# Kernel optimization log

Measured on AMD Instinct MI355X. Metric: run time of the kernel, lower is better.

## Reference

```python
import jax, jax.numpy as jnp
import numpy as np

NUM_ATOMS = 100
D = 32        # initial_atom_dim
H = 16        # hidden_dim (multiplicity per irrep)
NB = 16       # edge_dim / number of bessel basis functions
CUT = 6.0     # radius_cutoff
DEG = 4.0     # degree_norm
OUT = 1       # output_dim
INV4PI = 1.0 / np.sqrt(4.0 * np.pi)  # 'integral' SH normalization


def _bessel(d, nb, cut):
    # e3nn soft_one_hot_linspace(basis='bessel', cutoff=True) * sqrt(nb)
    x = d[:, None]
    n = jnp.arange(1, nb + 1, dtype=d.dtype)
    safe = jnp.maximum(x, 1e-9)
    out = np.sqrt(2.0 / cut) * jnp.sin(n * jnp.pi * x / cut) / safe
    return out * (x < cut) * np.sqrt(float(nb))


def _fc(x, w1, w2):
    # e3nn FullyConnectedNet: fan-in normalized linear layers, silu, no bias
    h = jax.nn.silu(x @ w1 / np.sqrt(x.shape[-1]))
    return h @ w2 / np.sqrt(w1.shape[-1])


def _forward(atomic_numbers, edge_index, coords, atom_emb,
             fc0_w1, fc0_w2, fc1_w1, fc1_w2, w_readout):
    src, dst = edge_index[0], edge_index[1]
    N = coords.shape[0]
    E = src.shape[0]

    vec = coords[src] - coords[dst]                      # [E,3]
    dist = jnp.linalg.norm(vec, axis=-1)                 # [E]
    unit = vec / jnp.maximum(dist, 1e-9)[:, None]

    # spherical harmonics, l=0 and l=1, 'integral' normalization
    y0 = jnp.full((E,), INV4PI, dtype=coords.dtype)      # [E]
    y1 = (np.sqrt(3.0) * INV4PI) * unit                  # [E,3]
    basis = _bessel(dist, NB, CUT)                       # [E,NB]

    x = atom_emb[atomic_numbers]                         # [N,D] (row 0 is padding)

    # ---- layer 0: scalars (D x0e) x (1x0e+1x1o) -> H x0e + H x1o ----
    w = _fc(basis, fc0_w1, fc0_w2)                       # [E, 2*D*H] per-edge TP weights
    wa = w[:, : D * H].reshape(E, D, H)
    wb = w[:, D * H:].reshape(E, D, H)
    xs = x[src]
    n0 = 1.0 / np.sqrt(D)                                # path fan-in norm
    m0 = jnp.einsum('ed,edh->eh', xs, wa) * y0[:, None] * n0          # [E,H]
    m1 = jnp.einsum('ed,edh->eh', xs, wb)[:, :, None] * y1[:, None, :] * n0  # [E,H,3]
    z0 = jax.ops.segment_sum(m0, dst, num_segments=N) / DEG           # [N,H]
    z1 = jax.ops.segment_sum(m1, dst, num_segments=N) / DEG           # [N,H,3]

    # ---- layer 1: (H x0e + H x1o) x (1x0e+1x1o) -> same irreps, skip-connected ----
    w = _fc(basis, fc1_w1, fc1_w2)                       # [E, 4*H*H]
    w1_ = w[:, 0 * H * H:1 * H * H].reshape(E, H, H)     # 0e x 0e -> 0e
    w2_ = w[:, 1 * H * H:2 * H * H].reshape(E, H, H)     # 0e x 1o -> 1o
    w3_ = w[:, 2 * H * H:3 * H * H].reshape(E, H, H)     # 1o x 0e -> 1o
    w4_ = w[:, 3 * H * H:4 * H * H].reshape(E, H, H)     # 1o x 1o -> 0e (CG = dot/sqrt(3))
    s, v = z0[src], z1[src]
    n1 = 1.0 / np.sqrt(2 * H)                            # two paths per output irrep
    dot = jnp.einsum('ehm,em->eh', v, y1) / np.sqrt(3.0)
    o0 = (jnp.einsum('eh,ehk->ek', s, w1_) * y0[:, None]
          + jnp.einsum('eh,ehk->ek', dot, w4_)) * n1
    o1 = (jnp.einsum('eh,ehk->ek', s, w2_)[:, :, None] * y1[:, None, :]
          + jnp.einsum('ehm,ehk->ekm', v, w3_) * y0[:, None, None]) * n1
    z0 = jax.ops.segment_sum(o0, dst, num_segments=N) / DEG + z0      # skip
    z1 = jax.ops.segment_sum(o1, dst, num_segments=N) / DEG + z1

    # ---- scalar readout (o3.Linear onto 0e) + graph sum-pool ----
    node_scalar = z0 @ w_readout / np.sqrt(H)            # [N,OUT]
    return jnp.sum(node_scalar, axis=0)                  # [OUT]


def setup_inputs() -> dict:
    key = jax.random.key(0)
    ks = jax.random.split(key, 9)
    N, E = 10000, 160000
    atomic_numbers = jax.random.randint(ks[0], (N,), 0, NUM_ATOMS)
    coords = jax.random.normal(ks[1], (N, 3), dtype=jnp.float32)
    edge_index = jax.random.randint(ks[2], (2, E), 0, N)
    atom_emb = jax.random.normal(ks[3], (NUM_ATOMS, D), dtype=jnp.float32).at[0].set(0.0)
    fc0_w1 = jax.random.normal(ks[4], (NB, H), dtype=jnp.float32)
    fc0_w2 = jax.random.normal(ks[5], (H, 2 * D * H), dtype=jnp.float32)
    fc1_w1 = jax.random.normal(ks[6], (NB, H), dtype=jnp.float32)
    fc1_w2 = jax.random.normal(ks[7], (H, 4 * H * H), dtype=jnp.float32)
    w_readout = jax.random.normal(ks[8], (H, OUT), dtype=jnp.float32)
    return {"atomic_numbers": atomic_numbers, "coords": coords, "edge_index": edge_index,
            "atom_emb": atom_emb, "fc0_w1": fc0_w1, "fc0_w2": fc0_w2,
            "fc1_w1": fc1_w1, "fc1_w2": fc1_w2, "w_readout": w_readout}


def reference(atomic_numbers, coords, edge_index, atom_emb,
              fc0_w1, fc0_w2, fc1_w1, fc1_w2, w_readout):
    return _forward(atomic_numbers, edge_index, coords, atom_emb,
                    fc0_w1, fc0_w2, fc1_w1, fc1_w2, w_readout)
```

## Files before the change

### kernel.cpp

```cpp
#include <hip/hip_runtime.h>
#include <math.h>


namespace {
constexpr int   NATOMS   = 100;
constexpr int   CAP      = 64;
constexpr float PI_F     = 3.14159265358979323846f;
constexpr float INV4PI_F = 0.28209479177387814f;
constexpr float SQRT3_F  = 1.7320508075688772f;
constexpr float CUT_F    = 6.0f;
constexpr float BASIS_C  = 2.3094010767585034f;
constexpr float N0_F     = 0.17677669529663687f;
constexpr float K0_F = INV4PI_F * N0_F * 0.0625f;
constexpr float K1_F = SQRT3_F * INV4PI_F * N0_F * 0.0625f;
constexpr float P2SC = INV4PI_F * N0_F * (1.0f / 64.0f);
}

__device__ __forceinline__ float silu_fast(float x) {
  return x / (1.0f + __expf(-x));
}

__device__ __forceinline__ float block_reduce_sum(float v) {
  #pragma unroll
  for (int o = 32; o > 0; o >>= 1) v += __shfl_down(v, o, 64);
  __shared__ float ls[8];
  int lane = threadIdx.x & 63;
  int w    = threadIdx.x >> 6;
  if (lane == 0) ls[w] = v;
  __syncthreads();
  float s = 0.f;
  if (threadIdx.x == 0) {
    int nw = (blockDim.x + 63) >> 6;
    for (int i = 0; i < nw; ++i) s += ls[i];
  }
  return s;
}

__global__ void table_kernel(const float* __restrict__ atom_emb,
                             const float* __restrict__ fc0_w2,
                             const float* __restrict__ fc1_w2,
                             const float* __restrict__ w_readout,
                             float* __restrict__ TI,
                             float* __restrict__ G1T, float* __restrict__ G4T,
                             int* __restrict__ dcur,
                             float* __restrict__ out,
                             int N2) {
  int b = blockIdx.x;
  int tt = threadIdx.x;
  if (b < NATOMS) {
    int j = tt >> 4;
    int h = tt & 15;
    float s0 = 0.f, s1 = 0.f;
    #pragma unroll
    for (int d = 0; d < 32; ++d) {
      float x = atom_emb[b * 32 + d];
      s0 = fmaf(x, fc0_w2[j * 1024 + d * 16 + h], s0);
      s1 = fmaf(x, fc0_w2[j * 1024 + 512 + d * 16 + h], s1);
    }
    TI[b * 512 + j * 32 + 2 * h]     = s0;
    TI[b * 512 + j * 32 + 2 * h + 1] = s1;
  } else if (b == NATOMS) {
    int j = tt >> 4;
    int h = tt & 15;
    float g1 = 0.f, g4 = 0.f;
    #pragma unroll
    for (int k = 0; k < 16; ++k) {
      float r = w_readout[k];
      g1 = fmaf(fc1_w2[j * 1024 + h * 16 + k], r, g1);
      g4 = fmaf(fc1_w2[j * 1024 + 768 + h * 16 + k], r, g4);
    }
    G1T[h * 16 + j] = g1;
    G4T[h * 16 + j] = g4;
    if (tt == 0) *out = 0.f;
  } else {
    int idx = (b - NATOMS - 1) * 256 + tt;
    if (idx < N2) dcur[idx] = 0;
  }
}

__global__ void __launch_bounds__(256)
edge_kernel(const int* __restrict__ ei,
            const float* __restrict__ coords,
            const int* __restrict__ an,
            const float* __restrict__ TI,
            const float* __restrict__ fc0_w1,
            const float* __restrict__ fc1_w1,
            int* __restrict__ dcur, int* __restrict__ scur,
            float2* __restrict__ mbuf,
            float4* __restrict__ ubuf,
            float4* __restrict__ sbuf,
            float* __restrict__ hbuf,
            int E) {
  int lane = threadIdx.x & 63;
  int g    = threadIdx.x >> 4;
  int t    = threadIdx.x & 15;
  int base = lane & 48;

  float w0c[16], w1c[16];
  #pragma unroll
  for (int k = 0; k < 16; ++k) {
    w0c[k] = fc0_w1[k * 16 + t];
    w1c[k] = fc1_w1[k * 16 + t];
  }

  const float angc = PI_F / CUT_F;
  int eA = blockIdx.x * 32 + g;
  int eB = eA + 16;
  bool vA = eA < E, vB = eB < E;
  int eAc = vA ? eA : 0, eBc = vB ? eB : 0;

  int sA = ei[eAc], dA = ei[E + eAc];
  int sB = ei[eBc], dB = ei[E + eBc];
  float sxA = coords[3 * sA + 0], syA = coords[3 * sA + 1], szA = coords[3 * sA + 2];
  float dxA = coords[3 * dA + 0], dyA = coords[3 * dA + 1], dzA = coords[3 * dA + 2];
  float sxB = coords[3 * sB + 0], syB = coords[3 * sB + 1], szB = coords[3 * sB + 2];
  float dxB = coords[3 * dB + 0], dyB = coords[3 * dB + 1], dzB = coords[3 * dB + 2];
  int aA = an[sA], aB = an[sB];

  float vxA = sxA - dxA, vyA = syA - dyA, vzA = szA - dzA;
  float vxB = sxB - dxB, vyB = syB - dyB, vzB = szB - dzB;
  float distA = sqrtf(vxA * vxA + vyA * vyA + vzA * vzA);
  float distB = sqrtf(vxB * vxB + vyB * vyB + vzB * vzB);
  float ivA = 1.0f / fmaxf(distA, 1e-9f);
  float ivB = 1.0f / fmaxf(distB, 1e-9f);
  float uxA = vxA * ivA, uyA = vyA * ivA, uzA = vzA * ivA;
  float uxB = vxB * ivB, uyB = vyB * ivB, uzB = vzB * ivB;
  float bcA = (distA < CUT_F) ? (BASIS_C * ivA) : 0.0f;
  float bcB = (distB < CUT_F) ? (BASIS_C * ivB) : 0.0f;

  int dsAv = 0, ssAv = 0, dsBv = 0, ssBv = 0;
  if (t == 0) {
    if (vA) {
      int p = atomicAdd(&dcur[dA], 1), q = atomicAdd(&scur[sA], 1);
      dsAv = dA * CAP + min(p, CAP - 1);
      ssAv = sA * CAP + min(q, CAP - 1);
      ubuf[dsAv] = make_float4(uxA, uyA, uzA, distA);
      sbuf[ssAv] = make_float4(uxA, uyA, uzA, distA);
    }
    if (vB) {
      int p = atomicAdd(&dcur[dB], 1), q = atomicAdd(&scur[sB], 1);
      dsBv = dB * CAP + min(p, CAP - 1);
      ssBv = sB * CAP + min(q, CAP - 1);
      ubuf[dsBv] = make_float4(uxB, uyB, uzB, distB);
      sbuf[ssBv] = make_float4(uxB, uyB, uzB, distB);
    }
  }

  float angA = angc * distA, angB = angc * distB;
  float scA = __sinf(angA), twA = 2.0f * __cosf(angA), spA = 0.f;
  float scB = __sinf(angB), twB = 2.0f * __cosf(angB), spB = 0.f;
  float a0A = 0.f, a1A = 0.f, a0B = 0.f, a1B = 0.f;
  #pragma unroll
  for (int k = 0; k < 16; ++k) {
    a0A = fmaf(scA, w0c[k], a0A);
    a1A = fmaf(scA, w1c[k], a1A);
    a0B = fmaf(scB, w0c[k], a0B);
    a1B = fmaf(scB, w1c[k], a1B);
    float snA = fmaf(twA, scA, -spA); spA = scA; scA = snA;
    float snB = fmaf(twB, scB, -spB); spB = scB; scB = snB;
  }
  float h0A = silu_fast(a0A * bcA * 0.25f);
  float h1A = silu_fast(a1A * bcA * 0.25f);
  float h0B = silu_fast(a0B * bcB * 0.25f);
  float h1B = silu_fast(a1B * bcB * 0.25f);

  int dsA = __shfl(dsAv, base, 64);
  int ssA = __shfl(ssAv, base, 64);
  int dsB = __shfl(dsBv, base, 64);
  int ssB = __shfl(ssBv, base, 64);

  const float2* tpA = (const float2*)(TI + aA * 512) + t;
  const float2* tpB = (const float2*)(TI + aB * 512) + t;
  float u0A = 0.f, u1A = 0.f, u0B = 0.f, u1B = 0.f;
  #pragma unroll
  for (int j = 0; j < 16; ++j) {
    float hjA = __shfl(h0A, base + j, 64);
    float hjB = __shfl(h0B, base + j, 64);
    float2 TA = tpA[j * 16];
    float2 TB = tpB[j * 16];
    u0A = fmaf(hjA, TA.x, u0A);
    u1A = fmaf(hjA, TA.y, u1A);
    u0B = fmaf(hjB, TB.x, u0B);
    u1B = fmaf(hjB, TB.y, u1B);
  }

  if (vA) {
    hbuf[(size_t)ssA * 16 + t] = h1A;
    mbuf[(size_t)dsA * 16 + t] = make_float2(K0_F * u0A, K1_F * u1A);
  }
  if (vB) {
    hbuf[(size_t)ssB * 16 + t] = h1B;
    mbuf[(size_t)dsB * 16 + t] = make_float2(K0_F * u0B, K1_F * u1B);
  }
}

__global__ void __launch_bounds__(256, 4)
node_kernel(const int* __restrict__ dcur,
            const int* __restrict__ scur,
            const float2* __restrict__ mbuf,
            const float4* __restrict__ ubuf,
            const float4* __restrict__ sbuf,
            const float* __restrict__ hbuf,
            const float* __restrict__ G1T,
            const float* __restrict__ G4T,
            const float* __restrict__ w_readout,
            float* __restrict__ out,
            int N) {
  __shared__ float ggs[512];
  ggs[threadIdx.x]       = G1T[threadIdx.x];
  ggs[256 + threadIdx.x] = G4T[threadIdx.x];
  __syncthreads();

  int wave = threadIdx.x >> 6;
  int lane = threadIdx.x & 63;
  int g    = lane >> 4;
  int t    = lane & 15;
  int base = lane & 48;
  int node = blockIdx.x * 4 + wave;
  bool valid = node < N;

  float rr = w_readout[t];
  int cin  = valid ? min(dcur[node], CAP) : 0;
  int cout = valid ? min(scur[node], CAP) : 0;
  size_t nb = (size_t)(valid ? node : 0) * CAP;

  float a0 = 0.f, ax = 0.f, ay = 0.f, az = 0.f;
  for (int i = g; i < cin; i += 4) {
    float2 f  = mbuf[(nb + i) * 16 + t];
    float4 uu = ubuf[nb + i];
    a0 += f.x;
    ax = fmaf(f.y, uu.x, ax);
    ay = fmaf(f.y, uu.y, ay);
    az = fmaf(f.y, uu.z, az);
  }
  a0 += __shfl_xor(a0, 16, 64); a0 += __shfl_xor(a0, 32, 64);
  ax += __shfl_xor(ax, 16, 64); ax += __shfl_xor(ax, 32, 64);
  ay += __shfl_xor(ay, 16, 64); ay += __shfl_xor(ay, 32, 64);
  az += __shfl_xor(az, 16, 64); az += __shfl_xor(az, 32, 64);

  float srcv = (g == 0) ? a0 : ((g == 1) ? ax : (g == 2) ? ay : az);
  int tofs = (g == 0) ? 0 : 256;
  float o = 0.f;
  #pragma unroll
  for (int h = 0; h < 16; ++h) {
    float vh = __shfl(srcv, base + h, 64);
    o = fmaf(ggs[tofs + h * 16 + t], vh, o);
  }
  float Qt  = __shfl(o, t, 64);
  float Pxt = __shfl(o, 16 + t, 64);
  float Pyt = __shfl(o, 32 + t, 64);
  float Pzt = __shfl(o, 48 + t, 64);

  float c = 0.f;
  for (int i = g; i < cout; i += 4) {
    float h1 = hbuf[(nb + i) * 16 + t];
    float4 uu = sbuf[nb + i];
    c = fmaf(h1, fmaf(Pxt, uu.x, fmaf(Pyt, uu.y, fmaf(Pzt, uu.z, Qt))), c);
  }
  c *= P2SC;
  if (valid && g == 0) c = fmaf(a0 * rr, 0.25f, c);
  if (!valid) c = 0.f;

  float tot = block_reduce_sum(c);
  if (threadIdx.x == 0) atomicAdd(out, tot);
}

extern "C" void kernel_launch(void* const* d_in, const int* in_sizes, int n_in,
                              void* d_out, int out_size, void* d_ws, size_t ws_size,
                              hipStream_t stream) {
  const int*   an        = (const int*)d_in[0];
  const float* coords    = (const float*)d_in[1];
  const int*   ei        = (const int*)d_in[2];
  const float* atom_emb  = (const float*)d_in[3];
  const float* fc0_w1    = (const float*)d_in[4];
  const float* fc0_w2    = (const float*)d_in[5];
  const float* fc1_w1    = (const float*)d_in[6];
  const float* fc1_w2    = (const float*)d_in[7];
  const float* w_readout = (const float*)d_in[8];

  int N = in_sizes[0];
  int E = in_sizes[2] / 2;
  size_t slots = (size_t)N * CAP;

  float4* ubuf = (float4*)d_ws;
  float4* sbuf = ubuf + slots;
  float2* mbuf = (float2*)(sbuf + slots);
  float*  hbuf = (float*)(mbuf + slots * 16);
  float*  TI   = hbuf + slots * 16;
  float*  G1T  = TI + NATOMS * 512;
  float*  G4T  = G1T + 256;
  int*    dcur = (int*)(G4T + 256);
  int*    scur = dcur + N;
  float*  out = (float*)d_out;

  int blk = 256;
  int zgrid = (2 * N + blk - 1) / blk;
  table_kernel<<<NATOMS + 1 + zgrid, blk, 0, stream>>>(
      atom_emb, fc0_w2, fc1_w2, w_readout, TI, G1T, G4T, dcur, out, 2 * N);

  edge_kernel<<<(E + 31) / 32, blk, 0, stream>>>(
      ei, coords, an, TI, fc0_w1, fc1_w1, dcur, scur,
      mbuf, ubuf, sbuf, hbuf, E);

  node_kernel<<<(N + 3) / 4, blk, 0, stream>>>(
      dcur, scur, mbuf, ubuf, sbuf, hbuf, G1T, G4T, w_readout, out, N);
}
```

Baseline: 148.6 us.

## Replace bucketed edge slots with float atomics and a separate edge readout pass

Drops the per-node fixed-capacity bucket lists built with integer atomic counters. Edge messages are now scatter-added straight into per-node accumulators with float atomics, and a new node kernel computes per-node Q/P vectors. A second edge pass then gathers those vectors by source index to form the readout. This removes the CAP=64 truncation and the large sparse slot buffers, at the cost of many more float atomics and an extra kernel launch with a random gather.

```diff
diff --git a/kernel.cpp b/kernel.cpp
--- a/kernel.cpp
+++ b/kernel.cpp
@@ -4,7 +4,6 @@
 
 namespace {
 constexpr int   NATOMS   = 100;
-constexpr int   CAP      = 64;
 constexpr float PI_F     = 3.14159265358979323846f;
 constexpr float INV4PI_F = 0.28209479177387814f;
 constexpr float SQRT3_F  = 1.7320508075688772f;
@@ -42,9 +41,9 @@
                              const float* __restrict__ w_readout,
                              float* __restrict__ TI,
                              float* __restrict__ G1T, float* __restrict__ G4T,
-                             int* __restrict__ dcur,
+                             float* __restrict__ zacc,
                              float* __restrict__ out,
-                             int N2) {
+                             int N64) {
   int b = blockIdx.x;
   int tt = threadIdx.x;
   if (b < NATOMS) {
@@ -74,7 +73,7 @@
     if (tt == 0) *out = 0.f;
   } else {
     int idx = (b - NATOMS - 1) * 256 + tt;
-    if (idx < N2) dcur[idx] = 0;
+    if (idx < N64) zacc[idx] = 0.f;
   }
 }
 
@@ -85,11 +84,9 @@
             const float* __restrict__ TI,
             const float* __restrict__ fc0_w1,
             const float* __restrict__ fc1_w1,
-            int* __restrict__ dcur, int* __restrict__ scur,
-            float2* __restrict__ mbuf,
+            float* __restrict__ zacc,
+            float* __restrict__ hbuf,
             float4* __restrict__ ubuf,
-            float4* __restrict__ sbuf,
-            float* __restrict__ hbuf,
             int E) {
   int lane = threadIdx.x & 63;
   int g    = threadIdx.x >> 4;
@@ -128,22 +125,9 @@
   float bcA = (distA < CUT_F) ? (BASIS_C * ivA) : 0.0f;
   float bcB = (distB < CUT_F) ? (BASIS_C * ivB) : 0.0f;
 
-  int dsAv = 0, ssAv = 0, dsBv = 0, ssBv = 0;
   if (t == 0) {
-    if (vA) {
-      int p = atomicAdd(&dcur[dA], 1), q = atomicAdd(&scur[sA], 1);
-      dsAv = dA * CAP + min(p, CAP - 1);
-      ssAv = sA * CAP + min(q, CAP - 1);
-      ubuf[dsAv] = make_float4(uxA, uyA, uzA, distA);
-      sbuf[ssAv] = make_float4(uxA, uyA, uzA, distA);
-    }
-    if (vB) {
-      int p = atomicAdd(&dcur[dB], 1), q = atomicAdd(&scur[sB], 1);
-      dsBv = dB * CAP + min(p, CAP - 1);
-      ssBv = sB * CAP + min(q, CAP - 1);
-      ubuf[dsBv] = make_float4(uxB, uyB, uzB, distB);
-      sbuf[ssBv] = make_float4(uxB, uyB, uzB, distB);
-    }
+    if (vA) ubuf[eA] = make_float4(uxA, uyA, uzA, 0.f);
+    if (vB) ubuf[eB] = make_float4(uxB, uyB, uzB, 0.f);
   }
 
   float angA = angc * distA, angB = angc * distB;
@@ -164,10 +148,8 @@
   float h0B = silu_fast(a0B * bcB * 0.25f);
   float h1B = silu_fast(a1B * bcB * 0.25f);
 
-  int dsA = __shfl(dsAv, base, 64);
-  int ssA = __shfl(ssAv, base, 64);
-  int dsB = __shfl(dsBv, base, 64);
-  int ssB = __shfl(ssBv, base, 64);
+  if (vA) hbuf[(size_t)eA * 16 + t] = h1A;
+  if (vB) hbuf[(size_t)eB * 16 + t] = h1B;
 
   const float2* tpA = (const float2*)(TI + aA * 512) + t;
   const float2* tpB = (const float2*)(TI + aB * 512) + t;
@@ -185,82 +167,98 @@
   }
 
   if (vA) {
-    hbuf[(size_t)ssA * 16 + t] = h1A;
-    mbuf[(size_t)dsA * 16 + t] = make_float2(K0_F * u0A, K1_F * u1A);
+    float* za = zacc + (size_t)dA * 64 + t;
+    float m1 = K1_F * u1A;
+    unsafeAtomicAdd(za,      K0_F * u0A);
+    unsafeAtomicAdd(za + 16, m1 * uxA);
+    unsafeAtomicAdd(za + 32, m1 * uyA);
+    unsafeAtomicAdd(za + 48, m1 * uzA);
   }
   if (vB) {
-    hbuf[(size_t)ssB * 16 + t] = h1B;
-    mbuf[(size_t)dsB * 16 + t] = make_float2(K0_F * u0B, K1_F * u1B);
-  }
-}
-
-__global__ void __launch_bounds__(256, 4)
-node_kernel(const int* __restrict__ dcur,
-            const int* __restrict__ scur,
-            const float2* __restrict__ mbuf,
-            const float4* __restrict__ ubuf,
-            const float4* __restrict__ sbuf,
-            const float* __restrict__ hbuf,
-            const float* __restrict__ G1T,
-            const float* __restrict__ G4T,
-            const float* __restrict__ w_readout,
-            float* __restrict__ out,
-            int N) {
+    float* zb = zacc + (size_t)dB * 64 + t;
+    float m1 = K1_F * u1B;
+    unsafeAtomicAdd(zb,      K0_F * u0B);
+    unsafeAtomicAdd(zb + 16, m1 * uxB);
+    unsafeAtomicAdd(zb + 32, m1 * uyB);
+    unsafeAtomicAdd(zb + 48, m1 * uzB);
+  }
+}
+
+__global__ void __launch_bounds__(256)
+node_qp_kernel(const float* __restrict__ zacc,
+               const float* __restrict__ G1T,
+               const float* __restrict__ G4T,
+               const float* __restrict__ w_readout,
+               float* __restrict__ QP,
+               float* __restrict__ out,
+               int N) {
   __shared__ float ggs[512];
   ggs[threadIdx.x]       = G1T[threadIdx.x];
   ggs[256 + threadIdx.x] = G4T[threadIdx.x];
   __syncthreads();
 
-  int wave = threadIdx.x >> 6;
   int lane = threadIdx.x & 63;
-  int g    = lane >> 4;
   int t    = lane & 15;
   int base = lane & 48;
-  int node = blockIdx.x * 4 + wave;
+  int node = blockIdx.x * 16 + (threadIdx.x >> 4);
   bool valid = node < N;
-
-  float rr = w_readout[t];
-  int cin  = valid ? min(dcur[node], CAP) : 0;
-  int cout = valid ? min(scur[node], CAP) : 0;
-  size_t nb = (size_t)(valid ? node : 0) * CAP;
-
-  float a0 = 0.f, ax = 0.f, ay = 0.f, az = 0.f;
-  for (int i = g; i < cin; i += 4) {
-    float2 f  = mbuf[(nb + i) * 16 + t];
-    float4 uu = ubuf[nb + i];
-    a0 += f.x;
-    ax = fmaf(f.y, uu.x, ax);
-    ay = fmaf(f.y, uu.y, ay);
-    az = fmaf(f.y, uu.z, az);
-  }
-  a0 += __shfl_xor(a0, 16, 64); a0 += __shfl_xor(a0, 32, 64);
-  ax += __shfl_xor(ax, 16, 64); ax += __shfl_xor(ax, 32, 64);
-  ay += __shfl_xor(ay, 16, 64); ay += __shfl_xor(ay, 32, 64);
-  az += __shfl_xor(az, 16, 64); az += __shfl_xor(az, 32, 64);
-
-  float srcv = (g == 0) ? a0 : ((g == 1) ? ax : (g == 2) ? ay : az);
-  int tofs = (g == 0) ? 0 : 256;
-  float o = 0.f;
+  size_t nb = (size_t)(valid ? node : 0) * 64;
+
+  float z0 = zacc[nb + t];
+  float zx = zacc[nb + 16 + t];
+  float zy = zacc[nb + 32 + t];
+  float zz = zacc[nb + 48 + t];
+
+  float Q = 0.f, Px = 0.f, Py = 0.f, Pz = 0.f;
   #pragma unroll
   for (int h = 0; h < 16; ++h) {
-    float vh = __shfl(srcv, base + h, 64);
-    o = fmaf(ggs[tofs + h * 16 + t], vh, o);
-  }
-  float Qt  = __shfl(o, t, 64);
-  float Pxt = __shfl(o, 16 + t, 64);
-  float Pyt = __shfl(o, 32 + t, 64);
-  float Pzt = __shfl(o, 48 + t, 64);
+    float z0h = __shfl(z0, base + h, 64);
+    float zxh = __shfl(zx, base + h, 64);
+    float zyh = __shfl(zy, base + h, 64);
+    float zzh = __shfl(zz, base + h, 64);
+    float g1 = ggs[h * 16 + t];
+    float g4 = ggs[256 + h * 16 + t];
+    Q  = fmaf(g1, z0h, Q);
+    Px = fmaf(g4, zxh, Px);
+    Py = fmaf(g4, zyh, Py);
+    Pz = fmaf(g4, zzh, Pz);
+  }
+  if (valid) {
+    QP[nb + t]      = Q;
+    QP[nb + 16 + t] = Px;
+    QP[nb + 32 + t] = Py;
+    QP[nb + 48 + t] = Pz;
+  }
+
+  float c = valid ? 0.25f * z0 * w_readout[t] : 0.f;
+  float tot = block_reduce_sum(c);
+  if (threadIdx.x == 0) atomicAdd(out, tot);
+}
+
+__global__ void __launch_bounds__(256)
+edge2_kernel(const int* __restrict__ ei,
+             const float4* __restrict__ ubuf,
+             const float* __restrict__ hbuf,
+             const float* __restrict__ QP,
+             float* __restrict__ out,
+             int E) {
+  int t  = threadIdx.x & 15;
+  int gg = blockIdx.x * 16 + (threadIdx.x >> 4);
+  int ngroups = gridDim.x * 16;
 
   float c = 0.f;
-  for (int i = g; i < cout; i += 4) {
-    float h1 = hbuf[(nb + i) * 16 + t];
-    float4 uu = sbuf[nb + i];
-    c = fmaf(h1, fmaf(Pxt, uu.x, fmaf(Pyt, uu.y, fmaf(Pzt, uu.z, Qt))), c);
+  for (int e = gg; e < E; e += ngroups) {
+    int s = ei[e];
+    float4 u = ubuf[e];
+    float h1 = hbuf[(size_t)e * 16 + t];
+    size_t sb = (size_t)s * 64;
+    float Qt  = QP[sb + t];
+    float Pxt = QP[sb + 16 + t];
+    float Pyt = QP[sb + 32 + t];
+    float Pzt = QP[sb + 48 + t];
+    c = fmaf(h1, fmaf(Pxt, u.x, fmaf(Pyt, u.y, fmaf(Pzt, u.z, Qt))), c);
   }
   c *= P2SC;
-  if (valid && g == 0) c = fmaf(a0 * rr, 0.25f, c);
-  if (!valid) c = 0.f;
-
   float tot = block_reduce_sum(c);
   if (threadIdx.x == 0) atomicAdd(out, tot);
 }
@@ -280,28 +278,27 @@
 
   int N = in_sizes[0];
   int E = in_sizes[2] / 2;
-  size_t slots = (size_t)N * CAP;
+  int N64 = N * 64;
 
   float4* ubuf = (float4*)d_ws;
-  float4* sbuf = ubuf + slots;
-  float2* mbuf = (float2*)(sbuf + slots);
-  float*  hbuf = (float*)(mbuf + slots * 16);
-  float*  TI   = hbuf + slots * 16;
+  float*  hbuf = (float*)(ubuf + E);
+  float*  zacc = hbuf + (size_t)E * 16;
+  float*  QP   = zacc + N64;
+  float*  TI   = QP + N64;
   float*  G1T  = TI + NATOMS * 512;
   float*  G4T  = G1T + 256;
-  int*    dcur = (int*)(G4T + 256);
-  int*    scur = dcur + N;
-  float*  out = (float*)d_out;
+  float*  out  = (float*)d_out;
 
   int blk = 256;
-  int zgrid = (2 * N + blk - 1) / blk;
+  int zgrid = (N64 + blk - 1) / blk;
   table_kernel<<<NATOMS + 1 + zgrid, blk, 0, stream>>>(
-      atom_emb, fc0_w2, fc1_w2, w_readout, TI, G1T, G4T, dcur, out, 2 * N);
+      atom_emb, fc0_w2, fc1_w2, w_readout, TI, G1T, G4T, zacc, out, N64);
 
   edge_kernel<<<(E + 31) / 32, blk, 0, stream>>>(
-      ei, coords, an, TI, fc0_w1, fc1_w1, dcur, scur,
-      mbuf, ubuf, sbuf, hbuf, E);
-
-  node_kernel<<<(N + 3) / 4, blk, 0, stream>>>(
-      dcur, scur, mbuf, ubuf, sbuf, hbuf, G1T, G4T, w_readout, out, N);
-}
+      ei, coords, an, TI, fc0_w1, fc1_w1, zacc, hbuf, ubuf, E);
+
+  node_qp_kernel<<<(N + 15) / 16, blk, 0, stream>>>(
+      zacc, G1T, G4T, w_readout, QP, out, N);
+
+  edge2_kernel<<<2048, blk, 0, stream>>>(ei, ubuf, hbuf, QP, out, E);
+}
```

Result: slower. 161.0 us (+8.4%).
